# Optimization experiments

Measured on AMD Instinct MI355X. Metric: run time of the kernel, lower is better.

## Reference

```python
import math
import jax, jax.numpy as jnp
import numpy as np

L, D, H, F = 4, 1024, 16, 4096
HD = D // H
EPS = 1e-5


def get_alibi_slopes(num_heads):
    closest = 2 ** math.floor(math.log2(num_heads))
    base = 2 ** (-2 ** (-(math.log2(closest) - 3)))
    slopes = base ** np.arange(1, closest + 1)
    if closest != num_heads:
        extra_base = 2 ** (-2 ** (-(math.log2(2 * closest) - 3)))
        extra = extra_base ** np.arange(1, 2 * (num_heads - closest) + 1, 2)
        slopes = np.concatenate([slopes, extra])
    return jnp.asarray(slopes, dtype=jnp.float32)


def build_mask(num_heads, T):
    # causal: -inf above diagonal; plus ALiBi slopes * (key_pos - query_pos)
    pos = jnp.arange(T)
    dist = pos[None, :] - pos[:, None]                      # (T, T)
    alibi = get_alibi_slopes(num_heads)[:, None, None] * dist[None]  # (H, T, T)
    causal = jnp.where(dist > 0, -jnp.inf, 0.0).astype(jnp.float32)
    return causal[None] + alibi                             # (H, T, T)


def layer_norm(x, w, b):
    mu = jnp.mean(x, axis=-1, keepdims=True)
    var = jnp.mean(jnp.square(x - mu), axis=-1, keepdims=True)
    return (x - mu) * jax.lax.rsqrt(var + EPS) * w + b


def mha(x, mask, Wi, bi, Wo, bo):
    B, T, _ = x.shape
    qkv = x @ Wi.T + bi                                     # (B, T, 3D)
    q, k, v = jnp.split(qkv, 3, axis=-1)
    q = q.reshape(B, T, H, HD).transpose(0, 2, 1, 3)        # (B, H, T, hd)
    k = k.reshape(B, T, H, HD).transpose(0, 2, 1, 3)
    v = v.reshape(B, T, H, HD).transpose(0, 2, 1, 3)
    scores = jnp.einsum('bhqd,bhkd->bhqk', q, k) / math.sqrt(HD)
    scores = scores + mask[None]                            # (B, H, T, T)
    attn = jax.nn.softmax(scores, axis=-1)
    out = jnp.einsum('bhqk,bhkd->bhqd', attn, v)
    out = out.transpose(0, 2, 1, 3).reshape(B, T, D)
    return out @ Wo.T + bo


def setup_inputs() -> dict:
    key = jax.random.key(0)
    ks = jax.random.split(key, 13)
    s = 0.02
    inp = {
        'x': jax.random.normal(ks[0], (2, 2048, D), dtype=jnp.float32),
        'in_proj_w': jax.random.normal(ks[1], (L, 3 * D, D), dtype=jnp.float32) * s,
        'in_proj_b': jnp.zeros((L, 3 * D), dtype=jnp.float32),
        'out_proj_w': jax.random.normal(ks[2], (L, D, D), dtype=jnp.float32) * s,
        'out_proj_b': jnp.zeros((L, D), dtype=jnp.float32),
        'ffn1_w': jax.random.normal(ks[3], (L, F, D), dtype=jnp.float32) * s,
        'ffn1_b': jnp.zeros((L, F), dtype=jnp.float32),
        'ffn2_w': jax.random.normal(ks[4], (L, D, F), dtype=jnp.float32) * s,
        'ffn2_b': jnp.zeros((L, D), dtype=jnp.float32),
        'ln1_w': jnp.ones((L, D), dtype=jnp.float32),
        'ln1_b': jnp.zeros((L, D), dtype=jnp.float32),
        'ln2_w': jnp.ones((L, D), dtype=jnp.float32),
        'ln2_b': jnp.zeros((L, D), dtype=jnp.float32),
        'final_w': jnp.ones((D,), dtype=jnp.float32),
        'final_b': jnp.zeros((D,), dtype=jnp.float32),
    }
    return inp


def reference(x, in_proj_w, in_proj_b, out_proj_w, out_proj_b,
              ffn1_w, ffn1_b, ffn2_w, ffn2_b,
              ln1_w, ln1_b, ln2_w, ln2_b, final_w, final_b):
    T = x.shape[1]
    mask = build_mask(H, T)                                 # (H, T, T)
    for i in range(L):
        xn = layer_norm(x, ln1_w[i], ln1_b[i])
        x = x + mha(xn, mask, in_proj_w[i], in_proj_b[i], out_proj_w[i], out_proj_b[i])
        xn = layer_norm(x, ln2_w[i], ln2_b[i])
        h = jax.nn.gelu(xn @ ffn1_w[i].T + ffn1_b[i], approximate=False)
        x = x + (h @ ffn2_w[i].T + ffn2_b[i])
    return layer_norm(x, final_w, final_b)
```

## Files before the change

### kernel.cpp

```cpp
#include <hip/hip_runtime.h>
#include <hip/hip_bf16.h>
#include <math.h>

typedef __bf16 bf16x8 __attribute__((ext_vector_type(8)));
typedef __bf16 bf16x4 __attribute__((ext_vector_type(4)));
typedef float  floatx4 __attribute__((ext_vector_type(4)));

#define D_MODEL 1024
#define SEQ     2048
#define NHEAD   16
#define HD      64

__device__ __forceinline__ void async16(const void* g, void* l) {
  __builtin_amdgcn_global_load_lds((const __attribute__((address_space(1))) void*)g,
                                   (__attribute__((address_space(3))) void*)l, 16, 0, 0);
}

__global__ __launch_bounds__(256)
void cvtw_kernel(const float* __restrict__ in, __bf16* __restrict__ out) {
  const size_t i = ((size_t)blockIdx.x * 256 + threadIdx.x) * 4;
  const floatx4 f = *(const floatx4*)(in + i);
  bf16x4 o = { (__bf16)f[0], (__bf16)f[1], (__bf16)f[2], (__bf16)f[3] };
  *(bf16x4*)(out + i) = o;
}

template<bool OUT_BF16>
__global__ __launch_bounds__(256)
void ln_kernel(const float* __restrict__ x, const float* __restrict__ w,
               const float* __restrict__ b, void* __restrict__ out)
{
  const int row = blockIdx.x;
  const int tid = threadIdx.x;
  const floatx4 f = *(const floatx4*)(x + (size_t)row * D_MODEL + tid * 4);
  float s = f[0] + f[1] + f[2] + f[3];
  #pragma unroll
  for (int off = 1; off < 64; off <<= 1) s += __shfl_xor(s, off);
  __shared__ float red[8];
  const int wv = tid >> 6;
  if ((tid & 63) == 0) red[wv] = s;
  __syncthreads();
  const float mu = (red[0] + red[1] + red[2] + red[3]) * (1.0f / 1024.0f);
  float d0 = f[0] - mu, d1 = f[1] - mu, d2 = f[2] - mu, d3 = f[3] - mu;
  float ss = d0 * d0 + d1 * d1 + d2 * d2 + d3 * d3;
  #pragma unroll
  for (int off = 1; off < 64; off <<= 1) ss += __shfl_xor(ss, off);
  if ((tid & 63) == 0) red[4 + wv] = ss;
  __syncthreads();
  const float rstd = rsqrtf((red[4] + red[5] + red[6] + red[7]) * (1.0f / 1024.0f) + 1e-5f);
  const floatx4 wv4 = *(const floatx4*)(w + tid * 4);
  const floatx4 bv4 = *(const floatx4*)(b + tid * 4);
  const float y0 = d0 * rstd * wv4[0] + bv4[0];
  const float y1 = d1 * rstd * wv4[1] + bv4[1];
  const float y2 = d2 * rstd * wv4[2] + bv4[2];
  const float y3 = d3 * rstd * wv4[3] + bv4[3];
  if (OUT_BF16) {
    bf16x4 o = { (__bf16)y0, (__bf16)y1, (__bf16)y2, (__bf16)y3 };
    *(bf16x4*)((__bf16*)out + (size_t)row * D_MODEL + tid * 4) = o;
  } else {
    floatx4 o = { y0, y1, y2, y3 };
    *(floatx4*)((float*)out + (size_t)row * D_MODEL + tid * 4) = o;
  }
}

#define EPI_GELU 1
#define EPI_RES  2
#define EPI_QKV  3

__device__ __forceinline__ void stage_q(int q, const __bf16* Ab, const __bf16* Wb,
                                        int K, int k0,
                                        __bf16 (*As)[64], __bf16 (*Bs)[64], int tid)
{
  #pragma unroll
  for (int j = 0; j < 2; ++j) {
    const int ch = j * 512 + tid;
    const int rq = ch >> 3, c16 = ch & 7;
    if (q == 0 || q == 3) {
      const int mh = (q == 3) ? 1 : 0;
      const int row = (rq & 63) + ((rq >> 6) << 7) + mh * 64;
      const int gc = (c16 ^ (row & 7)) * 8;
      async16(Ab + (size_t)row * K + k0 + gc, &As[row][c16 * 8]);
    } else {
      const int nh = (q == 2) ? 1 : 0;
      const int row = (rq & 31) + ((rq >> 5) << 6) + nh * 32;
      const int gc = (c16 ^ (row & 7)) * 8;
      async16(Wb + (size_t)row * K + k0 + gc, &Bs[row][c16 * 8]);
    }
  }
}

template<int MODE>
__global__ __launch_bounds__(512, 2)
void gemm256_kernel(const __bf16* __restrict__ A, const __bf16* __restrict__ W,
                    const float* __restrict__ bias, void* out,
                    __bf16* __restrict__ vT, int M, int N, int K)
{
  __shared__ __align__(16) __bf16 As[2][256][64];
  __shared__ __align__(16) __bf16 Bs[2][256][64];
  const int tid = threadIdx.x;
  const int lane = tid & 63, wv = tid >> 6;
  const int wr = wv >> 2, wc = wv & 3;
  const int quad = lane >> 4, r = lane & 15;
  const int sw = r & 7;
  const int m0 = blockIdx.x * 256, n0 = blockIdx.y * 256;
  const __bf16* Ab = A + (size_t)m0 * K;
  const __bf16* Wb = W + (size_t)n0 * K;

  floatx4 acc[8][4] = {};

  const int nt = K >> 6;
  stage_q(0, Ab, Wb, K, 0, As[0], Bs[0], tid);
  stage_q(1, Ab, Wb, K, 0, As[0], Bs[0], tid);
  stage_q(2, Ab, Wb, K, 0, As[0], Bs[0], tid);
  stage_q(3, Ab, Wb, K, 0, As[0], Bs[0], tid);

  for (int t = 0; t < nt; ++t) {
    const int p = t & 1;
    const int kn = (t + 1 < nt) ? ((t + 1) << 6) : 0;
    __bf16 (*Asr)[64] = As[p];
    __bf16 (*Bsr)[64] = Bs[p];
    __bf16 (*Asw)[64] = As[p ^ 1];
    __bf16 (*Bsw)[64] = Bs[p ^ 1];
    #pragma unroll
    for (int q = 0; q < 4; ++q) {
      stage_q(q, Ab, Wb, K, kn, Asw, Bsw, tid);
      if (q < 3) asm volatile("s_waitcnt vmcnt(6)" ::: "memory");
      __builtin_amdgcn_s_barrier();
      asm volatile("" ::: "memory");
      const int mh = q >> 1, nh = q & 1;
      __builtin_amdgcn_s_setprio(1);
      #pragma unroll
      for (int kk = 0; kk < 2; ++kk) {
        const int cc = ((kk * 4 + quad) ^ sw) * 8;
        bf16x8 av[4], bv[2];
        #pragma unroll
        for (int mi = 0; mi < 4; ++mi)
          av[mi] = *(const bf16x8*)&Asr[wr * 128 + mh * 64 + mi * 16 + r][cc];
        #pragma unroll
        for (int ni = 0; ni < 2; ++ni)
          bv[ni] = *(const bf16x8*)&Bsr[wc * 64 + nh * 32 + ni * 16 + r][cc];
        #pragma unroll
        for (int ni = 0; ni < 2; ++ni)
          #pragma unroll
          for (int mi = 0; mi < 4; ++mi)
            acc[mh * 4 + mi][nh * 2 + ni] = __builtin_amdgcn_mfma_f32_16x16x32_bf16(
                av[mi], bv[ni], acc[mh * 4 + mi][nh * 2 + ni], 0, 0, 0);
      }
      __builtin_amdgcn_s_setprio(0);
      asm volatile("" ::: "memory");
      __builtin_amdgcn_s_barrier();
    }
  }
  asm volatile("s_waitcnt vmcnt(0)" ::: "memory");

  #pragma unroll
  for (int ni = 0; ni < 4; ++ni) {
    const int nn = n0 + wc * 64 + ni * 16 + r;
    const float bvv = bias[nn];
    #pragma unroll
    for (int mi = 0; mi < 8; ++mi) {
      #pragma unroll
      for (int v = 0; v < 4; ++v) {
        const int mm = m0 + wr * 128 + mi * 16 + quad * 4 + v;
        float val = acc[mi][ni][v] + bvv;
        if (MODE == EPI_GELU) {
          val = 0.5f * val * (1.0f + erff(val * 0.70710678118654752f));
          ((__bf16*)out)[(size_t)mm * N + nn] = (__bf16)val;
        } else if (MODE == EPI_QKV) {
          if (nn < 2048) {
            const float sv = (nn < 1024) ? val * 0.125f : val;
            ((__bf16*)out)[(size_t)mm * 2048 + nn] = (__bf16)sv;
          } else {
            const int c = nn - 2048, hh = c >> 6, dd = c & 63;
            const int bb = mm >> 11, tt = mm & 2047;
            vT[(size_t)((bb * 16 + hh) * 64 + dd) * 2048 + tt] = (__bf16)val;
          }
        }
      }
    }
  }
}

__global__ __launch_bounds__(256, 2)
void gemm64_kernel(const __bf16* __restrict__ A, const __bf16* __restrict__ W,
                   const float* __restrict__ bias, float* __restrict__ out,
                   const float* __restrict__ res, int M, int N, int K)
{
  __shared__ __align__(16) __bf16 As0[128][32], As1[128][32];
  __shared__ __align__(16) __bf16 Ws0[64][32],  Ws1[64][32];
  const int tid = threadIdx.x;
  const int lane = tid & 63, w = tid >> 6;
  const int wr = w >> 1, wc = w & 1;
  const int quad = lane >> 4, r = lane & 15;
  const int m0 = blockIdx.x * 128, n0 = blockIdx.y * 64;

  floatx4 acc[4][2] = {};

  const __bf16* Ab = A + (size_t)m0 * K;
  const __bf16* Wb = W + (size_t)n0 * K;
  const int sr = tid >> 2, sc = (tid & 3) * 8;

  for (int k0 = 0; k0 < K; k0 += 64) {
    async16(Ab + (size_t)sr * K + k0 + sc,             &As0[sr][sc]);
    async16(Ab + (size_t)(sr + 64) * K + k0 + sc,      &As0[sr + 64][sc]);
    async16(Ab + (size_t)sr * K + k0 + 32 + sc,        &As1[sr][sc]);
    async16(Ab + (size_t)(sr + 64) * K + k0 + 32 + sc, &As1[sr + 64][sc]);
    async16(Wb + (size_t)sr * K + k0 + sc,             &Ws0[sr][sc]);
    async16(Wb + (size_t)sr * K + k0 + 32 + sc,        &Ws1[sr][sc]);
    __syncthreads();
    bf16x8 af0[4], af1[4];
    #pragma unroll
    for (int mi = 0; mi < 4; ++mi) {
      af0[mi] = *(const bf16x8*)&As0[wr * 64 + mi * 16 + r][quad * 8];
      af1[mi] = *(const bf16x8*)&As1[wr * 64 + mi * 16 + r][quad * 8];
    }
    #pragma unroll
    for (int ni = 0; ni < 2; ++ni) {
      const bf16x8 b0 = *(const bf16x8*)&Ws0[wc * 32 + ni * 16 + r][quad * 8];
      const bf16x8 b1 = *(const bf16x8*)&Ws1[wc * 32 + ni * 16 + r][quad * 8];
      #pragma unroll
      for (int mi = 0; mi < 4; ++mi) {
        acc[mi][ni] = __builtin_amdgcn_mfma_f32_16x16x32_bf16(af0[mi], b0, acc[mi][ni], 0, 0, 0);
        acc[mi][ni] = __builtin_amdgcn_mfma_f32_16x16x32_bf16(af1[mi], b1, acc[mi][ni], 0, 0, 0);
      }
    }
    __syncthreads();
  }

  #pragma unroll
  for (int ni = 0; ni < 2; ++ni) {
    const int nn = n0 + wc * 32 + ni * 16 + r;
    const float bv = bias[nn];
    #pragma unroll
    for (int mi = 0; mi < 4; ++mi) {
      #pragma unroll
      for (int v = 0; v < 4; ++v) {
        const int mm = m0 + wr * 64 + mi * 16 + quad * 4 + v;
        out[(size_t)mm * N + nn] = res[(size_t)mm * N + nn] + acc[mi][ni][v] + bv;
      }
    }
  }
}

template<int MODE, int NT>
__global__ __launch_bounds__(256, 2)
void gemm_legacy_kernel(const __bf16* __restrict__ A, const float* __restrict__ W,
                        const float* __restrict__ bias, void* out,
                        const float* __restrict__ res, __bf16* __restrict__ vT,
                        int M, int N, int K)
{
  __shared__ __align__(16) __bf16 As[128][32];
  __shared__ __align__(16) __bf16 Ws[NT][32];
  const int tid = threadIdx.x;
  const int lane = tid & 63, w = tid >> 6;
  const int wr = w >> 1, wc = w & 1;
  const int quad = lane >> 4, r = lane & 15;
  constexpr int NACC = NT / 32;
  const int m0 = blockIdx.x * 128, n0 = blockIdx.y * NT;
  floatx4 acc[4][NACC] = {};
  const __bf16* Ab = A + (size_t)m0 * K;
  const float*  Wb = W + (size_t)n0 * K;
  const int arow = tid >> 2, ac = (tid & 3) * 8;
  const int wrow = tid >> 3, wc4 = (tid & 7) * 4;
  for (int k0 = 0; k0 < K; k0 += 32) {
    async16(Ab + (size_t)arow * K + k0 + ac, &As[arow][ac]);
    async16(Ab + (size_t)(arow + 64) * K + k0 + ac, &As[arow + 64][ac]);
    #pragma unroll
    for (int i = 0; i < NT / 32; ++i) {
      const int rw = wrow + 32 * i;
      const floatx4 f = *(const floatx4*)(Wb + (size_t)rw * K + k0 + wc4);
      bf16x4 h4 = { (__bf16)f[0], (__bf16)f[1], (__bf16)f[2], (__bf16)f[3] };
      *(bf16x4*)&Ws[rw][wc4] = h4;
    }
    __syncthreads();
    bf16x8 af[4];
    #pragma unroll
    for (int mi = 0; mi < 4; ++mi)
      af[mi] = *(const bf16x8*)&As[wr * 64 + mi * 16 + r][quad * 8];
    #pragma unroll
    for (int ni = 0; ni < NACC; ++ni) {
      bf16x8 bf = *(const bf16x8*)&Ws[wc * (NT / 2) + ni * 16 + r][quad * 8];
      #pragma unroll
      for (int mi = 0; mi < 4; ++mi)
        acc[mi][ni] = __builtin_amdgcn_mfma_f32_16x16x32_bf16(af[mi], bf, acc[mi][ni], 0, 0, 0);
    }
    __syncthreads();
  }
  #pragma unroll
  for (int ni = 0; ni < NACC; ++ni) {
    const int nn = n0 + wc * (NT / 2) + ni * 16 + r;
    const float bv = bias[nn];
    #pragma unroll
    for (int mi = 0; mi < 4; ++mi) {
      #pragma unroll
      for (int v = 0; v < 4; ++v) {
        const int mm = m0 + wr * 64 + mi * 16 + quad * 4 + v;
        float val = acc[mi][ni][v] + bv;
        if (MODE == EPI_GELU) {
          val = 0.5f * val * (1.0f + erff(val * 0.70710678118654752f));
          ((__bf16*)out)[(size_t)mm * N + nn] = (__bf16)val;
        } else if (MODE == EPI_RES) {
          ((float*)out)[(size_t)mm * N + nn] = res[(size_t)mm * N + nn] + val;
        } else if (MODE == EPI_QKV) {
          if (nn < 2048) {
            const float sv = (nn < 1024) ? val * 0.125f : val;
            ((__bf16*)out)[(size_t)mm * 2048 + nn] = (__bf16)sv;
          } else {
            const int c = nn - 2048, hh = c >> 6, dd = c & 63;
            const int bb = mm >> 11, t = mm & 2047;
            vT[(size_t)((bb * 16 + hh) * 64 + dd) * 2048 + t] = (__bf16)val;
          }
        }
      }
    }
  }
}

__global__ __launch_bounds__(256, 4)
void attn_kernel(const __bf16* __restrict__ qk,
                 const __bf16* __restrict__ vT,
                 __bf16* __restrict__ out)
{
  __shared__ __align__(16) __bf16 Qs[2][64][32];
  __shared__ __align__(16) __bf16 Ks[2][64][32];
  __shared__ __align__(16) __bf16 Vs[2][64][32];
  __shared__ __align__(16) __bf16 Ps[4][2][16][32];
  const int tid = threadIdx.x, lane = tid & 63, w = tid >> 6;
  const int quad = lane >> 4, r = lane & 15;
  const int bh = blockIdx.x, b = bh >> 4, h = bh & 15;
  const int yk = blockIdx.y >> 3, yj = blockIdx.y & 7;
  const int qt = (yk << 3) | ((yk & 1) ? (7 - yj) : yj);
  const int q0 = qt * 64;

  {
    const __bf16* qb = qk + ((size_t)(b * SEQ + q0)) * 2048 + h * 64;
    #pragma unroll
    for (int rd = 0; rd < 2; ++rd) {
      const int c = rd * 256 + tid, half = c >> 8, row = (c >> 2) & 63, c8 = (c & 3) * 8;
      async16(qb + (size_t)row * 2048 + half * 32 + c8, &Qs[half][row][c8]);
    }
  }
  __syncthreads();
  const bf16x8 qf0 = *(const bf16x8*)&Qs[0][w * 16 + r][quad * 8];
  const bf16x8 qf1 = *(const bf16x8*)&Qs[1][w * 16 + r][quad * 8];

  const int q = q0 + w * 16 + r;
  float m_i = -INFINITY, l_i = 0.0f;
  floatx4 ot[4] = {};
  const float slope = exp2f(-0.5f * (float)(h + 1));
  const float sq = slope * (float)q;

  const __bf16* kb0 = qk + ((size_t)(b * SEQ)) * 2048 + 1024 + h * 64;
  const __bf16* vb0 = vT + ((size_t)(bh * 64)) * 2048;

  for (int kt = 0; kt <= qt; ++kt) {
    const int kbase = kt << 6;
    #pragma unroll
    for (int rd = 0; rd < 2; ++rd) {
      const int c = rd * 256 + tid, half = c >> 8, row = (c >> 2) & 63, c8 = (c & 3) * 8;
      async16(kb0 + (size_t)(kbase + row) * 2048 + half * 32 + c8, &Ks[half][row][c8]);
    }
    #pragma unroll
    for (int rd = 0; rd < 2; ++rd) {
      const int c = rd * 256 + tid, kb = c >> 8, d = (c >> 2) & 63, c8 = (c & 3) * 8;
      async16(vb0 + (size_t)d * 2048 + kbase + kb * 32 + c8, &Vs[kb][d][c8]);
    }
    __syncthreads();

    floatx4 st[4];
    #pragma unroll
    for (int t = 0; t < 4; ++t) {
      floatx4 z = { 0.0f, 0.0f, 0.0f, 0.0f };
      const bf16x8 kf0 = *(const bf16x8*)&Ks[0][t * 16 + r][quad * 8];
      const bf16x8 kf1 = *(const bf16x8*)&Ks[1][t * 16 + r][quad * 8];
      z = __builtin_amdgcn_mfma_f32_16x16x32_bf16(kf0, qf0, z, 0, 0, 0);
      st[t] = __builtin_amdgcn_mfma_f32_16x16x32_bf16(kf1, qf1, z, 0, 0, 0);
    }
    float mloc = -INFINITY;
    if (kt == qt) {
      #pragma unroll
      for (int t = 0; t < 4; ++t)
        #pragma unroll
        for (int v = 0; v < 4; ++v) {
          const int key = kbase + t * 16 + quad * 4 + v;
          float sv = st[t][v] + slope * (float)key - sq;
          sv = (key <= q) ? sv : -INFINITY;
          st[t][v] = sv;
          mloc = fmaxf(mloc, sv);
        }
    } else {
      #pragma unroll
      for (int t = 0; t < 4; ++t)
        #pragma unroll
        for (int v = 0; v < 4; ++v) {
          const int key = kbase + t * 16 + quad * 4 + v;
          const float sv = st[t][v] + slope * (float)key - sq;
          st[t][v] = sv;
          mloc = fmaxf(mloc, sv);
        }
    }
    mloc = fmaxf(mloc, __shfl_xor(mloc, 16));
    mloc = fmaxf(mloc, __shfl_xor(mloc, 32));
    const float mn = fmaxf(m_i, mloc);
    const float alpha = __expf(m_i - mn);
    m_i = mn;
    float rsum = 0.0f;
    #pragma unroll
    for (int t = 0; t < 4; ++t) {
      bf16x4 p4;
      #pragma unroll
      for (int v = 0; v < 4; ++v) {
        const float p = __expf(st[t][v] - mn);
        rsum += p;
        p4[v] = (__bf16)p;
      }
      *(bf16x4*)&Ps[w][t >> 1][r][(t & 1) * 16 + quad * 4] = p4;
    }
    rsum += __shfl_xor(rsum, 16);
    rsum += __shfl_xor(rsum, 32);
    l_i = l_i * alpha + rsum;
    #pragma unroll
    for (int dt = 0; dt < 4; ++dt) ot[dt] *= alpha;

    #pragma unroll
    for (int kb = 0; kb < 2; ++kb) {
      const bf16x8 pf = *(const bf16x8*)&Ps[w][kb][r][quad * 8];
      #pragma unroll
      for (int dt = 0; dt < 4; ++dt) {
        const bf16x8 vf = *(const bf16x8*)&Vs[kb][dt * 16 + r][quad * 8];
        ot[dt] = __builtin_amdgcn_mfma_f32_16x16x32_bf16(vf, pf, ot[dt], 0, 0, 0);
      }
    }
    __syncthreads();
  }

  const float linv = 1.0f / l_i;
  __bf16* ob = out + (size_t)(b * SEQ + q) * D_MODEL + h * 64;
  #pragma unroll
  for (int dt = 0; dt < 4; ++dt) {
    bf16x4 o4 = { (__bf16)(ot[dt][0] * linv), (__bf16)(ot[dt][1] * linv),
                  (__bf16)(ot[dt][2] * linv), (__bf16)(ot[dt][3] * linv) };
    *(bf16x4*)(ob + dt * 16 + quad * 4) = o4;
  }
}

extern "C" void kernel_launch(void* const* d_in, const int* in_sizes, int n_in,
                              void* d_out, int out_size, void* d_ws, size_t ws_size,
                              hipStream_t stream)
{
  (void)in_sizes; (void)n_in; (void)out_size;
  const float* x    = (const float*)d_in[0];
  const float* inW  = (const float*)d_in[1];
  const float* inB  = (const float*)d_in[2];
  const float* outW = (const float*)d_in[3];
  const float* outB = (const float*)d_in[4];
  const float* f1W  = (const float*)d_in[5];
  const float* f1B  = (const float*)d_in[6];
  const float* f2W  = (const float*)d_in[7];
  const float* f2B  = (const float*)d_in[8];
  const float* ln1W = (const float*)d_in[9];
  const float* ln1B = (const float*)d_in[10];
  const float* ln2W = (const float*)d_in[11];
  const float* ln2B = (const float*)d_in[12];
  const float* fnW  = (const float*)d_in[13];
  const float* fnB  = (const float*)d_in[14];

  char* ws = (char*)d_ws;
  float*  x_cur = (float*)(ws);
  __bf16* xn    = (__bf16*)(ws + 16777216);
  __bf16* qk    = (__bf16*)(ws + 25165824);
  __bf16* vT    = (__bf16*)(ws + 41943040);
  __bf16* attn  = (__bf16*)(ws + 50331648);
  __bf16* hbuf  = (__bf16*)(ws + 25165824);
  __bf16* inWb  = (__bf16*)(ws + 58720256);
  __bf16* outWb = (__bf16*)(ws + 83886080);
  __bf16* f1Wb  = (__bf16*)(ws + 92274688);
  __bf16* f2Wb  = (__bf16*)(ws + 125829120);
  const bool bf16w = ws_size >= (size_t)159383552;

  hipMemcpyAsync(x_cur, x, (size_t)16777216, hipMemcpyDeviceToDevice, stream);

  if (bf16w) {
    cvtw_kernel<<<dim3(12288), dim3(256), 0, stream>>>(inW,  inWb);
    cvtw_kernel<<<dim3(4096),  dim3(256), 0, stream>>>(outW, outWb);
    cvtw_kernel<<<dim3(16384), dim3(256), 0, stream>>>(f1W,  f1Wb);
    cvtw_kernel<<<dim3(16384), dim3(256), 0, stream>>>(f2W,  f2Wb);
  }

  for (int i = 0; i < 4; ++i) {
    ln_kernel<true><<<dim3(4096), dim3(256), 0, stream>>>(
        x_cur, ln1W + i * 1024, ln1B + i * 1024, xn);
    if (bf16w)
      gemm256_kernel<EPI_QKV><<<dim3(16, 12), dim3(512), 0, stream>>>(
          xn, inWb + (size_t)i * 3072 * 1024, inB + (size_t)i * 3072,
          qk, vT, 4096, 3072, 1024);
    else
      gemm_legacy_kernel<EPI_QKV, 128><<<dim3(32, 24), dim3(256), 0, stream>>>(
          xn, inW + (size_t)i * 3072 * 1024, inB + (size_t)i * 3072,
          qk, nullptr, vT, 4096, 3072, 1024);
    attn_kernel<<<dim3(32, 32), dim3(256), 0, stream>>>(qk, vT, attn);
    if (bf16w)
      gemm64_kernel<<<dim3(32, 16), dim3(256), 0, stream>>>(
          attn, outWb + (size_t)i * 1024 * 1024, outB + (size_t)i * 1024,
          x_cur, x_cur, 4096, 1024, 1024);
    else
      gemm_legacy_kernel<EPI_RES, 64><<<dim3(32, 16), dim3(256), 0, stream>>>(
          attn, outW + (size_t)i * 1024 * 1024, outB + (size_t)i * 1024,
          x_cur, x_cur, nullptr, 4096, 1024, 1024);
    ln_kernel<true><<<dim3(4096), dim3(256), 0, stream>>>(
        x_cur, ln2W + i * 1024, ln2B + i * 1024, xn);
    if (bf16w)
      gemm256_kernel<EPI_GELU><<<dim3(16, 16), dim3(512), 0, stream>>>(
          xn, f1Wb + (size_t)i * 4096 * 1024, f1B + (size_t)i * 4096,
          hbuf, nullptr, 4096, 4096, 1024);
    else
      gemm_legacy_kernel<EPI_GELU, 128><<<dim3(32, 32), dim3(256), 0, stream>>>(
          xn, f1W + (size_t)i * 4096 * 1024, f1B + (size_t)i * 4096,
          hbuf, nullptr, nullptr, 4096, 4096, 1024);
    if (bf16w)
      gemm64_kernel<<<dim3(32, 16), dim3(256), 0, stream>>>(
          hbuf, f2Wb + (size_t)i * 1024 * 4096, f2B + (size_t)i * 1024,
          x_cur, x_cur, 4096, 1024, 4096);
    else
      gemm_legacy_kernel<EPI_RES, 64><<<dim3(32, 16), dim3(256), 0, stream>>>(
          hbuf, f2W + (size_t)i * 1024 * 4096, f2B + (size_t)i * 1024,
          x_cur, x_cur, nullptr, 4096, 1024, 4096);
  }
  ln_kernel<false><<<dim3(4096), dim3(256), 0, stream>>>(x_cur, fnW, fnB, d_out);
}
```

Before: 1.494 ms.

## Replace quarter-tile staged pipeline with whole-tile double buffering in GEMM

The GEMM main loop previously split each K-tile's loads and MFMA work into four quarter phases, each with its own barriers. Now it issues the whole next tile's async loads at once, waits for the current tile, and runs all 32 MFMAs per kk step between two barriers. This cuts the barrier count per K-tile and enlarges the MFMA batches. In exchange it gives up the fine-grained overlap of loads with compute, and each wave holds more fragment registers at once.

```diff
diff --git a/kernel.cpp b/kernel.cpp
--- a/kernel.cpp
+++ b/kernel.cpp
@@ -66,25 +66,23 @@
 #define EPI_RES  2
 #define EPI_QKV  3
 
-__device__ __forceinline__ void stage_q(int q, const __bf16* Ab, const __bf16* Wb,
-                                        int K, int k0,
-                                        __bf16 (*As)[64], __bf16 (*Bs)[64], int tid)
-{
-  #pragma unroll
-  for (int j = 0; j < 2; ++j) {
+__device__ __forceinline__ void stage_tile(const __bf16* Ab, const __bf16* Wb,
+                                           int K, int k0,
+                                           __bf16 (*As)[64], __bf16 (*Bs)[64], int tid)
+{
+  #pragma unroll
+  for (int j = 0; j < 4; ++j) {
     const int ch = j * 512 + tid;
-    const int rq = ch >> 3, c16 = ch & 7;
-    if (q == 0 || q == 3) {
-      const int mh = (q == 3) ? 1 : 0;
-      const int row = (rq & 63) + ((rq >> 6) << 7) + mh * 64;
-      const int gc = (c16 ^ (row & 7)) * 8;
-      async16(Ab + (size_t)row * K + k0 + gc, &As[row][c16 * 8]);
-    } else {
-      const int nh = (q == 2) ? 1 : 0;
-      const int row = (rq & 31) + ((rq >> 5) << 6) + nh * 32;
-      const int gc = (c16 ^ (row & 7)) * 8;
-      async16(Wb + (size_t)row * K + k0 + gc, &Bs[row][c16 * 8]);
-    }
+    const int row = ch >> 3, c16 = ch & 7;
+    const int gc = (c16 ^ (row & 7)) * 8;
+    async16(Ab + (size_t)row * K + k0 + gc, &As[row][c16 * 8]);
+  }
+  #pragma unroll
+  for (int j = 0; j < 4; ++j) {
+    const int ch = j * 512 + tid;
+    const int row = ch >> 3, c16 = ch & 7;
+    const int gc = (c16 ^ (row & 7)) * 8;
+    async16(Wb + (size_t)row * K + k0 + gc, &Bs[row][c16 * 8]);
   }
 }
 
@@ -108,47 +106,38 @@
   floatx4 acc[8][4] = {};
 
   const int nt = K >> 6;
-  stage_q(0, Ab, Wb, K, 0, As[0], Bs[0], tid);
-  stage_q(1, Ab, Wb, K, 0, As[0], Bs[0], tid);
-  stage_q(2, Ab, Wb, K, 0, As[0], Bs[0], tid);
-  stage_q(3, Ab, Wb, K, 0, As[0], Bs[0], tid);
+  stage_tile(Ab, Wb, K, 0, As[0], Bs[0], tid);
 
   for (int t = 0; t < nt; ++t) {
     const int p = t & 1;
     const int kn = (t + 1 < nt) ? ((t + 1) << 6) : 0;
+    stage_tile(Ab, Wb, K, kn, As[p ^ 1], Bs[p ^ 1], tid);
+    asm volatile("s_waitcnt vmcnt(8)" ::: "memory");
+    __builtin_amdgcn_s_barrier();
+    asm volatile("" ::: "memory");
     __bf16 (*Asr)[64] = As[p];
     __bf16 (*Bsr)[64] = Bs[p];
-    __bf16 (*Asw)[64] = As[p ^ 1];
-    __bf16 (*Bsw)[64] = Bs[p ^ 1];
-    #pragma unroll
-    for (int q = 0; q < 4; ++q) {
-      stage_q(q, Ab, Wb, K, kn, Asw, Bsw, tid);
-      if (q < 3) asm volatile("s_waitcnt vmcnt(6)" ::: "memory");
-      __builtin_amdgcn_s_barrier();
-      asm volatile("" ::: "memory");
-      const int mh = q >> 1, nh = q & 1;
+    #pragma unroll
+    for (int kk = 0; kk < 2; ++kk) {
+      const int cc = ((kk * 4 + quad) ^ sw) * 8;
+      bf16x8 av[8], bv[4];
+      #pragma unroll
+      for (int mi = 0; mi < 8; ++mi)
+        av[mi] = *(const bf16x8*)&Asr[wr * 128 + mi * 16 + r][cc];
+      #pragma unroll
+      for (int ni = 0; ni < 4; ++ni)
+        bv[ni] = *(const bf16x8*)&Bsr[wc * 64 + ni * 16 + r][cc];
       __builtin_amdgcn_s_setprio(1);
       #pragma unroll
-      for (int kk = 0; kk < 2; ++kk) {
-        const int cc = ((kk * 4 + quad) ^ sw) * 8;
-        bf16x8 av[4], bv[2];
+      for (int ni = 0; ni < 4; ++ni)
         #pragma unroll
-        for (int mi = 0; mi < 4; ++mi)
-          av[mi] = *(const bf16x8*)&Asr[wr * 128 + mh * 64 + mi * 16 + r][cc];
-        #pragma unroll
-        for (int ni = 0; ni < 2; ++ni)
-          bv[ni] = *(const bf16x8*)&Bsr[wc * 64 + nh * 32 + ni * 16 + r][cc];
-        #pragma unroll
-        for (int ni = 0; ni < 2; ++ni)
-          #pragma unroll
-          for (int mi = 0; mi < 4; ++mi)
-            acc[mh * 4 + mi][nh * 2 + ni] = __builtin_amdgcn_mfma_f32_16x16x32_bf16(
-                av[mi], bv[ni], acc[mh * 4 + mi][nh * 2 + ni], 0, 0, 0);
-      }
+        for (int mi = 0; mi < 8; ++mi)
+          acc[mi][ni] = __builtin_amdgcn_mfma_f32_16x16x32_bf16(
+              av[mi], bv[ni], acc[mi][ni], 0, 0, 0);
       __builtin_amdgcn_s_setprio(0);
-      asm volatile("" ::: "memory");
-      __builtin_amdgcn_s_barrier();
-    }
+    }
+    asm volatile("" ::: "memory");
+    __builtin_amdgcn_s_barrier();
   }
   asm volatile("s_waitcnt vmcnt(0)" ::: "memory");
 
```

Result: faster. 1.350 ms (-9.7%).
